# Kernel optimization log

Measured on AMD Instinct MI355X. Metric: run time of the kernel, lower is better.

The kernel has to match this reference:

```python
import jax, jax.numpy as jnp
import numpy as np

M = 2048
K = 512


def setup_inputs() -> dict:
    key = jax.random.key(0)
    k1, k2, k3, k4, k5 = jax.random.split(key, 5)
    inputs = jax.random.normal(k1, (16384, M), dtype=jnp.float32)
    # MyLinear(m, k): weight [k, m], bias [k] (torch Linear convention)
    s1 = 1.0 / np.sqrt(M)
    s2 = 1.0 / np.sqrt(K)
    W1 = jax.random.uniform(k2, (K, M), jnp.float32, -s1, s1)
    b1 = jax.random.uniform(k3, (K,), jnp.float32, -s1, s1)
    W2 = jax.random.uniform(k4, (M, K), jnp.float32, -s2, s2)
    b2 = jax.random.uniform(k5, (M,), jnp.float32, -s2, s2)
    return {"inputs": inputs, "W1": W1, "b1": b1, "W2": W2, "b2": b2}


def reference(inputs, W1, b1, W2, b2):
    # Original loops per sample; math is identical to one batched chain:
    # hidden = x @ W1^T + b1 ; out = hidden @ W2^T + b2 (no nonlinearity)
    hidden = jnp.einsum("bm,km->bk", inputs, W1) + b1  # [B, K]
    out = jnp.einsum("bk,mk->bm", hidden, W2) + b2     # [B, M]
    return out
```

## Files before the change

kernel.cpp:

```cpp
#include <hip/hip_runtime.h>
#include <hip/hip_bf16.h>
#include <stdint.h>


typedef short bf16x8 __attribute__((ext_vector_type(8)));
typedef float f32x4 __attribute__((ext_vector_type(4)));

static __device__ __forceinline__ unsigned short f32_to_bf16_rne(float f) {
    unsigned int u = __float_as_uint(f);
    u += 0x7fffu + ((u >> 16) & 1u);
    return (unsigned short)(u >> 16);
}

static __device__ __forceinline__ unsigned int cvt_pk_bf16(float lo, float hi) {
    unsigned int r;
    asm("v_cvt_pk_bf16_f32 %0, %1, %2" : "=v"(r) : "v"(lo), "v"(hi));
    return r;
}

__global__ void cast_weights_bf16(const float* __restrict__ w1,
                                  unsigned short* __restrict__ o1,
                                  const float* __restrict__ w2,
                                  unsigned short* __restrict__ o2, int n4each) {
    int stride = gridDim.x * blockDim.x;
    for (int i = blockIdx.x * blockDim.x + threadIdx.x; i < 2 * n4each;
         i += stride) {
        const float* in = (i < n4each) ? w1 : w2;
        unsigned short* out = (i < n4each) ? o1 : o2;
        int j = (i < n4each) ? i : i - n4each;
        float4 v = ((const float4*)in)[j];
        ushort4 o;
        o.x = f32_to_bf16_rne(v.x);
        o.y = f32_to_bf16_rne(v.y);
        o.z = f32_to_bf16_rne(v.z);
        o.w = f32_to_bf16_rne(v.w);
        ((ushort4*)out)[j] = o;
    }
}

#define GLOAD_LDS16(gsrc, ldst)                                              \
    __builtin_amdgcn_global_load_lds(                                        \
        (const __attribute__((address_space(1))) void*)(gsrc),               \
        (__attribute__((address_space(3))) void*)(ldst), 16, 0, 0)

__global__ __launch_bounds__(256, 2)
void gemm1_xcast(const float* __restrict__ X,
                 const unsigned short* __restrict__ W1,
                 const float* __restrict__ b1,
                 unsigned short* __restrict__ H) {
    constexpr int K = 2048, N = 512, BK = 64, NSTEP = K / BK;

    __shared__ __align__(16) float ldsX[128 * BK];
    __shared__ __align__(16) unsigned short ldsW[128 * BK];

    const int tid  = threadIdx.x;
    const int lane = tid & 63;
    const int wid  = tid >> 6;
    const int wr   = wid >> 1;
    const int wc   = wid & 1;

    const int bid = blockIdx.x;
    const int swz = ((bid & 7) << 6) + (bid >> 3);
    const int bm  = swz >> 2;
    const int bn  = swz & 3;
    const int brow = bm << 7;
    const int bcol = bn << 7;

    const int lrow = lane & 15;
    const int ku   = lane >> 4;

    const int xr  = tid >> 4;
    const int xsw = ((tid & 15) ^ xr) << 4;
    const char* xsrc0 = (const char*)(X + (size_t)(brow + xr) * K) + xsw;

    const int wrr = tid >> 3;
    const int wsw = ((tid & 7) ^ (wrr & 7)) << 4;
    const char* wsrc0 = (const char*)(W1 + (size_t)(bcol + wrr) * K) + wsw;

    f32x4 acc[4][4] = {};

    auto stage = [&](int k0) {
#pragma unroll
        for (int i = 0; i < 8; ++i)
            GLOAD_LDS16(xsrc0 + ((size_t)i * 16 * K + k0) * 4,
                        (char*)ldsX + i * 4096 + tid * 16);
#pragma unroll
        for (int i = 0; i < 4; ++i)
            GLOAD_LDS16(wsrc0 + ((size_t)i * 32 * K + k0) * 2,
                        (char*)ldsW + i * 4096 + tid * 16);
    };

    auto compute = [&]() {
#pragma unroll
        for (int kk = 0; kk < 2; ++kk) {
            const int luA = (ku + (kk << 2)) << 1;
            const int unW = ((ku + (kk << 2)) ^ (lrow & 7)) << 4;
            bf16x8 a[4], b[4];
#pragma unroll
            for (int m = 0; m < 4; ++m) {
                const int ra = (wr << 6) + (m << 4) + lrow;
                const char* base = (const char*)ldsX + ra * 256;
                f32x4 lo = *(const f32x4*)(base + ((luA ^ lrow) << 4));
                f32x4 hi = *(const f32x4*)(base + (((luA + 1) ^ lrow) << 4));
                uint4 u;
                u.x = cvt_pk_bf16(lo[0], lo[1]);
                u.y = cvt_pk_bf16(lo[2], lo[3]);
                u.z = cvt_pk_bf16(hi[0], hi[1]);
                u.w = cvt_pk_bf16(hi[2], hi[3]);
                a[m] = *(const bf16x8*)&u;
            }
#pragma unroll
            for (int n = 0; n < 4; ++n)
                b[n] = *(const bf16x8*)((const char*)ldsW +
                       ((wc << 6) + (n << 4) + lrow) * 128 + unW);
#pragma unroll
            for (int m = 0; m < 4; ++m)
#pragma unroll
                for (int n = 0; n < 4; ++n)
                    acc[m][n] = __builtin_amdgcn_mfma_f32_16x16x32_bf16(
                        a[m], b[n], acc[m][n], 0, 0, 0);
        }
    };

    stage(0);
    __syncthreads();

    for (int t = 0; t < NSTEP; ++t) {
        compute();
        if (t + 1 < NSTEP) {
            __syncthreads();
            stage((t + 1) * BK);
            __syncthreads();
        }
    }

    const int r0 = (lane >> 4) << 2;
#pragma unroll
    for (int n = 0; n < 4; ++n) {
        const int col = bcol + (wc << 6) + (n << 4) + lrow;
        const float bb = b1[col];
#pragma unroll
        for (int m = 0; m < 4; ++m)
#pragma unroll
            for (int j = 0; j < 4; ++j) {
                const int row = brow + (wr << 6) + (m << 4) + r0 + j;
                H[(size_t)row * N + col] = f32_to_bf16_rne(acc[m][n][j] + bb);
            }
    }
}

__global__ __launch_bounds__(256)
void gemm2(const unsigned short* __restrict__ A,
           const unsigned short* __restrict__ Bt,
           const float* __restrict__ bias,
           float* __restrict__ C) {
    constexpr int N = 2048, Kd = 512, BK = 64, NSTEP = Kd / BK;

    __shared__ __align__(16) unsigned short ldsA[128 * BK];
    __shared__ __align__(16) unsigned short ldsB[128 * BK];

    const int tid  = threadIdx.x;
    const int lane = tid & 63;
    const int wid  = tid >> 6;
    const int wr   = wid >> 1;
    const int wc   = wid & 1;

    const int bid = blockIdx.x;
    const int swz = ((bid & 7) << 8) + (bid >> 3);
    const int bn  = swz & 15;
    const int bm  = swz >> 4;
    const int brow = bm << 7;
    const int bcol = bn << 7;

    const int lrow = lane & 15;
    const int ku   = lane >> 4;
    const int rx   = lrow & 7;

    const int srow = tid >> 3;
    const int sgu  = (tid & 7) ^ (srow & 7);

    f32x4 acc[4][4] = {};

    auto stage = [&](int k0) {
#pragma unroll
        for (int i = 0; i < 4; ++i) {
            const int row = i * 32 + srow;
            const char* sa =
                (const char*)(A + (size_t)(brow + row) * Kd + k0) + (sgu << 4);
            const char* sb =
                (const char*)(Bt + (size_t)(bcol + row) * Kd + k0) + (sgu << 4);
            GLOAD_LDS16(sa, (char*)ldsA + i * 4096 + tid * 16);
            GLOAD_LDS16(sb, (char*)ldsB + i * 4096 + tid * 16);
        }
    };
    auto compute = [&]() {
#pragma unroll
        for (int kk = 0; kk < 2; ++kk) {
            const int un = ((ku + (kk << 2)) ^ rx) << 4;
            bf16x8 a[4], b[4];
#pragma unroll
            for (int m = 0; m < 4; ++m)
                a[m] = *(const bf16x8*)((const char*)ldsA +
                       ((wr << 6) + (m << 4) + lrow) * 128 + un);
#pragma unroll
            for (int n = 0; n < 4; ++n)
                b[n] = *(const bf16x8*)((const char*)ldsB +
                       ((wc << 6) + (n << 4) + lrow) * 128 + un);
#pragma unroll
            for (int m = 0; m < 4; ++m)
#pragma unroll
                for (int n = 0; n < 4; ++n)
                    acc[m][n] = __builtin_amdgcn_mfma_f32_16x16x32_bf16(
                        a[m], b[n], acc[m][n], 0, 0, 0);
        }
    };

    stage(0);
    __syncthreads();

    for (int t = 0; t < NSTEP; ++t) {
        compute();
        if (t + 1 < NSTEP) {
            __syncthreads();
            stage((t + 1) * BK);
            __syncthreads();
        }
    }

    const int r0 = (lane >> 4) << 2;
#pragma unroll
    for (int n = 0; n < 4; ++n) {
        const int col = bcol + (wc << 6) + (n << 4) + lrow;
        const float bb = bias[col];
#pragma unroll
        for (int m = 0; m < 4; ++m)
#pragma unroll
            for (int j = 0; j < 4; ++j) {
                const int row = brow + (wr << 6) + (m << 4) + r0 + j;
                C[(size_t)row * N + col] = acc[m][n][j] + bb;
            }
    }
}

extern "C" void kernel_launch(void* const* d_in, const int* in_sizes, int n_in,
                              void* d_out, int out_size, void* d_ws, size_t ws_size,
                              hipStream_t stream) {
    const float* X  = (const float*)d_in[0];
    const float* W1 = (const float*)d_in[1];
    const float* b1 = (const float*)d_in[2];
    const float* W2 = (const float*)d_in[3];
    const float* b2 = (const float*)d_in[4];

    const int B = 16384, M = 2048, Kd = 512;

    char* ws = (char*)d_ws;
    unsigned short* W1bf = (unsigned short*)ws;
    unsigned short* W2bf = W1bf + (size_t)Kd * M;
    unsigned short* Hbf  = W2bf + (size_t)M * Kd;

    cast_weights_bf16<<<2048, 256, 0, stream>>>(W1, W1bf, W2, W2bf,
                                                Kd * M / 4);

    gemm1_xcast<<<(B / 128) * (Kd / 128), 256, 0, stream>>>(X, W1bf, b1, Hbf);
    gemm2<<<(B / 128) * (M / 128), 256, 0, stream>>>(Hbf, W2bf, b2,
                                                     (float*)d_out);
}
```

Measured before the change: 126.6 us.

## Triple-buffer LDS in gemm1 with async global-to-LDS prefetch two tiles ahead

Restructures the first GEMM's main loop from a single LDS buffer with load-then-compute into a three-stage ring of buffers. Tiles are prefetched two steps ahead with direct global-to-LDS loads, gated by explicit vmcnt waits and raw barriers. BK is halved to 32 to fit three buffers, the swizzles are adjusted to match, MFMA sections get raised s_setprio, and the occupancy hint of 2 blocks per CU is dropped. The goal is to hide global load latency behind MFMA work, at the cost of more barriers per unit of K and possibly lower occupancy.

```diff
diff --git a/kernel.cpp b/kernel.cpp
--- a/kernel.cpp
+++ b/kernel.cpp
@@ -43,15 +43,15 @@
         (const __attribute__((address_space(1))) void*)(gsrc),               \
         (__attribute__((address_space(3))) void*)(ldst), 16, 0, 0)
 
-__global__ __launch_bounds__(256, 2)
+__global__ __launch_bounds__(256)
 void gemm1_xcast(const float* __restrict__ X,
                  const unsigned short* __restrict__ W1,
                  const float* __restrict__ b1,
                  unsigned short* __restrict__ H) {
-    constexpr int K = 2048, N = 512, BK = 64, NSTEP = K / BK;
-
-    __shared__ __align__(16) float ldsX[128 * BK];
-    __shared__ __align__(16) unsigned short ldsW[128 * BK];
+    constexpr int K = 2048, N = 512, BK = 32, NSTEP = K / BK;
+    constexpr int BUFB = 24576, WOFF = 16384;
+
+    __shared__ __align__(16) char lds3[3][BUFB];
 
     const int tid  = threadIdx.x;
     const int lane = tid & 63;
@@ -69,69 +69,77 @@
     const int lrow = lane & 15;
     const int ku   = lane >> 4;
 
-    const int xr  = tid >> 4;
-    const int xsw = ((tid & 15) ^ xr) << 4;
-    const char* xsrc0 = (const char*)(X + (size_t)(brow + xr) * K) + xsw;
-
-    const int wrr = tid >> 3;
-    const int wsw = ((tid & 7) ^ (wrr & 7)) << 4;
-    const char* wsrc0 = (const char*)(W1 + (size_t)(bcol + wrr) * K) + wsw;
+    const char* xsrc0 = (const char*)(X + (size_t)(brow + (tid >> 3)) * K) +
+                        (((tid & 7) ^ ((tid >> 3) & 7)) << 4);
+    const char* wsrc0 = (const char*)(W1 + (size_t)(bcol + (tid >> 2)) * K) +
+                        (((tid & 3) ^ ((tid >> 2) & 3)) << 4);
 
     f32x4 acc[4][4] = {};
 
-    auto stage = [&](int k0) {
-#pragma unroll
-        for (int i = 0; i < 8; ++i)
-            GLOAD_LDS16(xsrc0 + ((size_t)i * 16 * K + k0) * 4,
-                        (char*)ldsX + i * 4096 + tid * 16);
+    auto stage = [&](int k0, char* buf) {
 #pragma unroll
         for (int i = 0; i < 4; ++i)
-            GLOAD_LDS16(wsrc0 + ((size_t)i * 32 * K + k0) * 2,
-                        (char*)ldsW + i * 4096 + tid * 16);
-    };
-
-    auto compute = [&]() {
-#pragma unroll
-        for (int kk = 0; kk < 2; ++kk) {
-            const int luA = (ku + (kk << 2)) << 1;
-            const int unW = ((ku + (kk << 2)) ^ (lrow & 7)) << 4;
-            bf16x8 a[4], b[4];
-#pragma unroll
-            for (int m = 0; m < 4; ++m) {
-                const int ra = (wr << 6) + (m << 4) + lrow;
-                const char* base = (const char*)ldsX + ra * 256;
-                f32x4 lo = *(const f32x4*)(base + ((luA ^ lrow) << 4));
-                f32x4 hi = *(const f32x4*)(base + (((luA + 1) ^ lrow) << 4));
-                uint4 u;
-                u.x = cvt_pk_bf16(lo[0], lo[1]);
-                u.y = cvt_pk_bf16(lo[2], lo[3]);
-                u.z = cvt_pk_bf16(hi[0], hi[1]);
-                u.w = cvt_pk_bf16(hi[2], hi[3]);
-                a[m] = *(const bf16x8*)&u;
-            }
+            GLOAD_LDS16(xsrc0 + ((size_t)i * 32 * K + k0) * 4,
+                        buf + i * 4096 + tid * 16);
+#pragma unroll
+        for (int i = 0; i < 2; ++i)
+            GLOAD_LDS16(wsrc0 + ((size_t)i * 64 * K + k0) * 2,
+                        buf + WOFF + i * 4096 + tid * 16);
+    };
+
+    auto compute = [&](const char* buf) {
+        const char* bW = buf + WOFF;
+        bf16x8 a[4], b[4];
+#pragma unroll
+        for (int m = 0; m < 4; ++m) {
+            const int ra = (wr << 6) + (m << 4) + lrow;
+            const char* base = buf + ra * 128;
+            f32x4 lo = *(const f32x4*)(base + (((ku << 1) ^ (lrow & 7)) << 4));
+            f32x4 hi = *(const f32x4*)(base + ((((ku << 1) | 1) ^ (lrow & 7)) << 4));
+            uint4 u;
+            u.x = cvt_pk_bf16(lo[0], lo[1]);
+            u.y = cvt_pk_bf16(lo[2], lo[3]);
+            u.z = cvt_pk_bf16(hi[0], hi[1]);
+            u.w = cvt_pk_bf16(hi[2], hi[3]);
+            a[m] = *(const bf16x8*)&u;
+        }
+#pragma unroll
+        for (int n = 0; n < 4; ++n) {
+            const int rb = (wc << 6) + (n << 4) + lrow;
+            b[n] = *(const bf16x8*)(bW + rb * 64 + ((ku ^ (lrow & 3)) << 4));
+        }
+        __builtin_amdgcn_s_setprio(1);
+#pragma unroll
+        for (int m = 0; m < 4; ++m)
 #pragma unroll
             for (int n = 0; n < 4; ++n)
-                b[n] = *(const bf16x8*)((const char*)ldsW +
-                       ((wc << 6) + (n << 4) + lrow) * 128 + unW);
-#pragma unroll
-            for (int m = 0; m < 4; ++m)
-#pragma unroll
-                for (int n = 0; n < 4; ++n)
-                    acc[m][n] = __builtin_amdgcn_mfma_f32_16x16x32_bf16(
-                        a[m], b[n], acc[m][n], 0, 0, 0);
-        }
-    };
-
-    stage(0);
-    __syncthreads();
-
+                acc[m][n] = __builtin_amdgcn_mfma_f32_16x16x32_bf16(
+                    a[m], b[n], acc[m][n], 0, 0, 0);
+        __builtin_amdgcn_s_setprio(0);
+    };
+
+    stage(0, lds3[0]);
+    stage(BK, lds3[1]);
+    char* cb0 = lds3[0];
+    char* cb1 = lds3[1];
+    char* cb2 = lds3[2];
+
+#pragma unroll 1
     for (int t = 0; t < NSTEP; ++t) {
-        compute();
-        if (t + 1 < NSTEP) {
-            __syncthreads();
-            stage((t + 1) * BK);
-            __syncthreads();
-        }
+        if (t + 2 < NSTEP) {
+            stage((t + 2) * BK, cb2);
+            asm volatile("s_waitcnt vmcnt(12)" ::: "memory");
+        } else if (t + 2 == NSTEP) {
+            asm volatile("s_waitcnt vmcnt(6)" ::: "memory");
+        } else {
+            asm volatile("s_waitcnt vmcnt(0)" ::: "memory");
+        }
+        __builtin_amdgcn_s_barrier();
+        asm volatile("" ::: "memory");
+        compute(cb0);
+        asm volatile("" ::: "memory");
+        __builtin_amdgcn_s_barrier();
+        char* tmp = cb0; cb0 = cb1; cb1 = cb2; cb2 = tmp;
     }
 
     const int r0 = (lane >> 4) << 2;
```

After: 137.3 us. +8.5%, slower.

## Pre-cast X to bf16 in a separate pass and use a pure bf16 GEMM1

Applied to the files above, without the earlier changes.

Extends the weight-cast kernel to also convert the large fp32 input X to bf16 in workspace, and replaces the fused fp32-load-and-convert GEMM1 with a plain bf16 GEMM that mirrors GEMM2. This removes in-kernel fp32 LDS traffic and conversion work and halves GEMM1's LDS footprint. In exchange it adds a full extra pass over X (read fp32, write bf16, reread bf16), increasing global memory traffic.

```diff
diff --git a/kernel.cpp b/kernel.cpp
--- a/kernel.cpp
+++ b/kernel.cpp
@@ -12,22 +12,25 @@
     return (unsigned short)(u >> 16);
 }
 
-static __device__ __forceinline__ unsigned int cvt_pk_bf16(float lo, float hi) {
-    unsigned int r;
-    asm("v_cvt_pk_bf16_f32 %0, %1, %2" : "=v"(r) : "v"(lo), "v"(hi));
-    return r;
-}
-
-__global__ void cast_weights_bf16(const float* __restrict__ w1,
-                                  unsigned short* __restrict__ o1,
-                                  const float* __restrict__ w2,
-                                  unsigned short* __restrict__ o2, int n4each) {
-    int stride = gridDim.x * blockDim.x;
-    for (int i = blockIdx.x * blockDim.x + threadIdx.x; i < 2 * n4each;
-         i += stride) {
-        const float* in = (i < n4each) ? w1 : w2;
-        unsigned short* out = (i < n4each) ? o1 : o2;
-        int j = (i < n4each) ? i : i - n4each;
+__global__ void cast_bf16_all(const float* __restrict__ x,
+                              unsigned short* __restrict__ xo, int nx4,
+                              const float* __restrict__ w1,
+                              unsigned short* __restrict__ w1o,
+                              const float* __restrict__ w2,
+                              unsigned short* __restrict__ w2o, int nw4) {
+    const int total = nx4 + 2 * nw4;
+    const int stride = gridDim.x * blockDim.x;
+    for (int i = blockIdx.x * blockDim.x + threadIdx.x; i < total; i += stride) {
+        const float* in;
+        unsigned short* out;
+        int j;
+        if (i < nx4) {
+            in = x; out = xo; j = i;
+        } else if (i < nx4 + nw4) {
+            in = w1; out = w1o; j = i - nx4;
+        } else {
+            in = w2; out = w2o; j = i - nx4 - nw4;
+        }
         float4 v = ((const float4*)in)[j];
         ushort4 o;
         o.x = f32_to_bf16_rne(v.x);
@@ -43,15 +46,15 @@
         (const __attribute__((address_space(1))) void*)(gsrc),               \
         (__attribute__((address_space(3))) void*)(ldst), 16, 0, 0)
 
-__global__ __launch_bounds__(256, 2)
-void gemm1_xcast(const float* __restrict__ X,
-                 const unsigned short* __restrict__ W1,
-                 const float* __restrict__ b1,
-                 unsigned short* __restrict__ H) {
-    constexpr int K = 2048, N = 512, BK = 64, NSTEP = K / BK;
-
-    __shared__ __align__(16) float ldsX[128 * BK];
-    __shared__ __align__(16) unsigned short ldsW[128 * BK];
+__global__ __launch_bounds__(256)
+void gemm1_bf(const unsigned short* __restrict__ A,
+              const unsigned short* __restrict__ Bt,
+              const float* __restrict__ bias,
+              unsigned short* __restrict__ H) {
+    constexpr int N = 512, Kd = 2048, BK = 64, NSTEP = Kd / BK;
+
+    __shared__ __align__(16) unsigned short ldsA[128 * BK];
+    __shared__ __align__(16) unsigned short ldsB[128 * BK];
 
     const int tid  = threadIdx.x;
     const int lane = tid & 63;
@@ -63,112 +66,6 @@
     const int swz = ((bid & 7) << 6) + (bid >> 3);
     const int bm  = swz >> 2;
     const int bn  = swz & 3;
-    const int brow = bm << 7;
-    const int bcol = bn << 7;
-
-    const int lrow = lane & 15;
-    const int ku   = lane >> 4;
-
-    const int xr  = tid >> 4;
-    const int xsw = ((tid & 15) ^ xr) << 4;
-    const char* xsrc0 = (const char*)(X + (size_t)(brow + xr) * K) + xsw;
-
-    const int wrr = tid >> 3;
-    const int wsw = ((tid & 7) ^ (wrr & 7)) << 4;
-    const char* wsrc0 = (const char*)(W1 + (size_t)(bcol + wrr) * K) + wsw;
-
-    f32x4 acc[4][4] = {};
-
-    auto stage = [&](int k0) {
-#pragma unroll
-        for (int i = 0; i < 8; ++i)
-            GLOAD_LDS16(xsrc0 + ((size_t)i * 16 * K + k0) * 4,
-                        (char*)ldsX + i * 4096 + tid * 16);
-#pragma unroll
-        for (int i = 0; i < 4; ++i)
-            GLOAD_LDS16(wsrc0 + ((size_t)i * 32 * K + k0) * 2,
-                        (char*)ldsW + i * 4096 + tid * 16);
-    };
-
-    auto compute = [&]() {
-#pragma unroll
-        for (int kk = 0; kk < 2; ++kk) {
-            const int luA = (ku + (kk << 2)) << 1;
-            const int unW = ((ku + (kk << 2)) ^ (lrow & 7)) << 4;
-            bf16x8 a[4], b[4];
-#pragma unroll
-            for (int m = 0; m < 4; ++m) {
-                const int ra = (wr << 6) + (m << 4) + lrow;
-                const char* base = (const char*)ldsX + ra * 256;
-                f32x4 lo = *(const f32x4*)(base + ((luA ^ lrow) << 4));
-                f32x4 hi = *(const f32x4*)(base + (((luA + 1) ^ lrow) << 4));
-                uint4 u;
-                u.x = cvt_pk_bf16(lo[0], lo[1]);
-                u.y = cvt_pk_bf16(lo[2], lo[3]);
-                u.z = cvt_pk_bf16(hi[0], hi[1]);
-                u.w = cvt_pk_bf16(hi[2], hi[3]);
-                a[m] = *(const bf16x8*)&u;
-            }
-#pragma unroll
-            for (int n = 0; n < 4; ++n)
-                b[n] = *(const bf16x8*)((const char*)ldsW +
-                       ((wc << 6) + (n << 4) + lrow) * 128 + unW);
-#pragma unroll
-            for (int m = 0; m < 4; ++m)
-#pragma unroll
-                for (int n = 0; n < 4; ++n)
-                    acc[m][n] = __builtin_amdgcn_mfma_f32_16x16x32_bf16(
-                        a[m], b[n], acc[m][n], 0, 0, 0);
-        }
-    };
-
-    stage(0);
-    __syncthreads();
-
-    for (int t = 0; t < NSTEP; ++t) {
-        compute();
-        if (t + 1 < NSTEP) {
-            __syncthreads();
-            stage((t + 1) * BK);
-            __syncthreads();
-        }
-    }
-
-    const int r0 = (lane >> 4) << 2;
-#pragma unroll
-    for (int n = 0; n < 4; ++n) {
-        const int col = bcol + (wc << 6) + (n << 4) + lrow;
-        const float bb = b1[col];
-#pragma unroll
-        for (int m = 0; m < 4; ++m)
-#pragma unroll
-            for (int j = 0; j < 4; ++j) {
-                const int row = brow + (wr << 6) + (m << 4) + r0 + j;
-                H[(size_t)row * N + col] = f32_to_bf16_rne(acc[m][n][j] + bb);
-            }
-    }
-}
-
-__global__ __launch_bounds__(256)
-void gemm2(const unsigned short* __restrict__ A,
-           const unsigned short* __restrict__ Bt,
-           const float* __restrict__ bias,
-           float* __restrict__ C) {
-    constexpr int N = 2048, Kd = 512, BK = 64, NSTEP = Kd / BK;
-
-    __shared__ __align__(16) unsigned short ldsA[128 * BK];
-    __shared__ __align__(16) unsigned short ldsB[128 * BK];
-
-    const int tid  = threadIdx.x;
-    const int lane = tid & 63;
-    const int wid  = tid >> 6;
-    const int wr   = wid >> 1;
-    const int wc   = wid & 1;
-
-    const int bid = blockIdx.x;
-    const int swz = ((bid & 7) << 8) + (bid >> 3);
-    const int bn  = swz & 15;
-    const int bm  = swz >> 4;
     const int brow = bm << 7;
     const int bcol = bn << 7;
 
@@ -218,6 +115,100 @@
     stage(0);
     __syncthreads();
 
+#pragma unroll 1
+    for (int t = 0; t < NSTEP; ++t) {
+        compute();
+        if (t + 1 < NSTEP) {
+            __syncthreads();
+            stage((t + 1) * BK);
+            __syncthreads();
+        }
+    }
+
+    const int r0 = (lane >> 4) << 2;
+#pragma unroll
+    for (int n = 0; n < 4; ++n) {
+        const int col = bcol + (wc << 6) + (n << 4) + lrow;
+        const float bb = bias[col];
+#pragma unroll
+        for (int m = 0; m < 4; ++m)
+#pragma unroll
+            for (int j = 0; j < 4; ++j) {
+                const int row = brow + (wr << 6) + (m << 4) + r0 + j;
+                H[(size_t)row * N + col] = f32_to_bf16_rne(acc[m][n][j] + bb);
+            }
+    }
+}
+
+__global__ __launch_bounds__(256)
+void gemm2(const unsigned short* __restrict__ A,
+           const unsigned short* __restrict__ Bt,
+           const float* __restrict__ bias,
+           float* __restrict__ C) {
+    constexpr int N = 2048, Kd = 512, BK = 64, NSTEP = Kd / BK;
+
+    __shared__ __align__(16) unsigned short ldsA[128 * BK];
+    __shared__ __align__(16) unsigned short ldsB[128 * BK];
+
+    const int tid  = threadIdx.x;
+    const int lane = tid & 63;
+    const int wid  = tid >> 6;
+    const int wr   = wid >> 1;
+    const int wc   = wid & 1;
+
+    const int bid = blockIdx.x;
+    const int swz = ((bid & 7) << 8) + (bid >> 3);
+    const int bn  = swz & 15;
+    const int bm  = swz >> 4;
+    const int brow = bm << 7;
+    const int bcol = bn << 7;
+
+    const int lrow = lane & 15;
+    const int ku   = lane >> 4;
+    const int rx   = lrow & 7;
+
+    const int srow = tid >> 3;
+    const int sgu  = (tid & 7) ^ (srow & 7);
+
+    f32x4 acc[4][4] = {};
+
+    auto stage = [&](int k0) {
+#pragma unroll
+        for (int i = 0; i < 4; ++i) {
+            const int row = i * 32 + srow;
+            const char* sa =
+                (const char*)(A + (size_t)(brow + row) * Kd + k0) + (sgu << 4);
+            const char* sb =
+                (const char*)(Bt + (size_t)(bcol + row) * Kd + k0) + (sgu << 4);
+            GLOAD_LDS16(sa, (char*)ldsA + i * 4096 + tid * 16);
+            GLOAD_LDS16(sb, (char*)ldsB + i * 4096 + tid * 16);
+        }
+    };
+    auto compute = [&]() {
+#pragma unroll
+        for (int kk = 0; kk < 2; ++kk) {
+            const int un = ((ku + (kk << 2)) ^ rx) << 4;
+            bf16x8 a[4], b[4];
+#pragma unroll
+            for (int m = 0; m < 4; ++m)
+                a[m] = *(const bf16x8*)((const char*)ldsA +
+                       ((wr << 6) + (m << 4) + lrow) * 128 + un);
+#pragma unroll
+            for (int n = 0; n < 4; ++n)
+                b[n] = *(const bf16x8*)((const char*)ldsB +
+                       ((wc << 6) + (n << 4) + lrow) * 128 + un);
+#pragma unroll
+            for (int m = 0; m < 4; ++m)
+#pragma unroll
+                for (int n = 0; n < 4; ++n)
+                    acc[m][n] = __builtin_amdgcn_mfma_f32_16x16x32_bf16(
+                        a[m], b[n], acc[m][n], 0, 0, 0);
+        }
+    };
+
+    stage(0);
+    __syncthreads();
+
     for (int t = 0; t < NSTEP; ++t) {
         compute();
         if (t + 1 < NSTEP) {
@@ -257,11 +248,15 @@
     unsigned short* W1bf = (unsigned short*)ws;
     unsigned short* W2bf = W1bf + (size_t)Kd * M;
     unsigned short* Hbf  = W2bf + (size_t)M * Kd;
-
-    cast_weights_bf16<<<2048, 256, 0, stream>>>(W1, W1bf, W2, W2bf,
-                                                Kd * M / 4);
-
-    gemm1_xcast<<<(B / 128) * (Kd / 128), 256, 0, stream>>>(X, W1bf, b1, Hbf);
+    unsigned short* Xbf  = Hbf + (size_t)B * Kd;
+
+    const int nx4 = B * M / 4;
+    const int nw4 = Kd * M / 4;
+
+    cast_bf16_all<<<4096, 256, 0, stream>>>(X, Xbf, nx4, W1, W1bf, W2, W2bf,
+                                            nw4);
+
+    gemm1_bf<<<(B / 128) * (Kd / 128), 256, 0, stream>>>(Xbf, W1bf, b1, Hbf);
     gemm2<<<(B / 128) * (M / 128), 256, 0, stream>>>(Hbf, W2bf, b2,
                                                      (float*)d_out);
 }
```

After: 136.1 us. 1.07x slower.
